# Performance work log

Hardware: AMD Instinct MI355X
Metric: run time of the kernel (lower is better)

The kernel has to match this reference:

```python
import jax, jax.numpy as jnp
import numpy as np

N = 50000   # nodes
E = 800000  # edges
H = 128     # hidden_dim
K = 4       # Chebyshev order
EPS_BN = 1e-5
EPS_L2 = 1e-12


def setup_inputs() -> dict:
    key = jax.random.key(0)
    ks = jax.random.split(key, 8)
    x = jax.random.normal(ks[0], (N, 3), dtype=jnp.float32)
    edge_index = jax.random.randint(ks[1], (2, E), 0, N, dtype=jnp.int32)

    def lin(k, fi, fo):
        s = 1.0 / np.sqrt(fi)
        return jax.random.uniform(k, (fi, fo), jnp.float32, -s, s)

    def cheb_params(k, fi, fo):
        kk = jax.random.split(k, K)
        W = jnp.stack([lin(kk[i], fi, fo) for i in range(K)])  # [K, fi, fo]
        b = jnp.zeros((fo,), jnp.float32)
        return W, b

    W1, b1 = cheb_params(ks[2], 3, H)
    W2, b2 = cheb_params(ks[3], H, H)
    W3, b3 = cheb_params(ks[4], H, H)
    W4, b4 = cheb_params(ks[5], H, H)
    Wr = lin(ks[6], H, 3)
    br = jnp.zeros((3,), jnp.float32)
    ones = jnp.ones((H,), jnp.float32)
    zeros = jnp.zeros((H,), jnp.float32)
    return {
        'x': x, 'edge_index': edge_index,
        'W1': W1, 'b1': b1, 'W2': W2, 'b2': b2,
        'W3': W3, 'b3': b3, 'W4': W4, 'b4': b4,
        'g1': ones, 'be1': zeros, 'g2': ones, 'be2': zeros,
        'g3': ones, 'be3': zeros, 'Wr': Wr, 'br': br,
    }


def _prop(h, src, dst, norm):
    # one sparse Laplacian application: out[dst] += norm * h[src]
    return jax.ops.segment_sum(norm[:, None] * h[src], dst, num_segments=N)


def _cheb(h, src, dst, norm, W, b):
    # PyG ChebConv with sym normalization, lambda_max=2 -> L_hat edge weights
    # are -D^-1/2 A D^-1/2 with zero diagonal (encoded in norm).
    out = h @ W[0]
    Tx0, Tx1 = h, _prop(h, src, dst, norm)
    out = out + Tx1 @ W[1]
    for k in range(2, W.shape[0]):
        Tx2 = 2.0 * _prop(Tx1, src, dst, norm) - Tx0
        out = out + Tx2 @ W[k]
        Tx0, Tx1 = Tx1, Tx2
    return out + b


def _bn(h, g, b):
    # BatchNorm1d in training mode: batch stats over node dim, biased var
    m = h.mean(axis=0)
    v = h.var(axis=0)
    return g * (h - m) * jax.lax.rsqrt(v + EPS_BN) + b


def reference(x, edge_index, W1, b1, W2, b2, W3, b3, W4, b4,
              g1, be1, g2, be2, g3, be3, Wr, br):
    src, dst = edge_index[0], edge_index[1]
    deg = jax.ops.segment_sum(jnp.ones((E,), jnp.float32), src, num_segments=N)
    dinv = jnp.where(deg > 0, jax.lax.rsqrt(jnp.maximum(deg, 1.0)), 0.0)
    norm = -dinv[src] * dinv[dst]

    h = _bn(jax.nn.leaky_relu(_cheb(x, src, dst, norm, W1, b1)), g1, be1)
    h = _bn(jax.nn.leaky_relu(_cheb(h, src, dst, norm, W2, b2)), g2, be2)
    h = _bn(jax.nn.relu(_cheb(h, src, dst, norm, W3, b3)), g3, be3)
    h = _cheb(h, src, dst, norm, W4, b4)
    # F.normalize(p=2, dim=1)
    h = h / jnp.maximum(jnp.linalg.norm(h, axis=1, keepdims=True), EPS_L2)
    return h @ Wr + br
```

## Files before the change

### kernel.cpp

```cpp
#include <hip/hip_runtime.h>
#include <hip/hip_fp16.h>

#define HD 128

typedef __attribute__((ext_vector_type(8))) _Float16 f16x8;
typedef __attribute__((ext_vector_type(4))) float f32x4;
typedef unsigned int u32;

struct h4s { __half2 a, b; };
struct h8s { __half2 a, b, c, d; };

__device__ __forceinline__ float lrelu(float x, float s) { return x > 0.f ? x : s * x; }

__device__ __forceinline__ float2 bn_coeff(const float* st, const float* g,
                                           const float* be, float invn, int f) {
  float m = st[f] * invn;
  float v = st[HD + f] * invn - m * m;
  float sc = g[f] * rsqrtf(v + 1e-5f);
  return make_float2(sc, be[f] - m * sc);
}

__global__ void k_edge_count(const int* __restrict__ src, const int* __restrict__ dst,
                             int* __restrict__ degc, int* __restrict__ cnt,
                             int* __restrict__ ledge, int E) {
  int e = blockIdx.x * blockDim.x + threadIdx.x;
  if (e < E) {
    atomicAdd(&degc[src[e]], 1);
    ledge[e] = atomicAdd(&cnt[dst[e]], 1);
  }
}

__global__ __launch_bounds__(1024) void k_scan1(const int* __restrict__ cnt,
                                                int* __restrict__ rowptr,
                                                int* __restrict__ bsums,
                                                float* __restrict__ stats, int n) {
  if (blockIdx.x == 0 && threadIdx.x < 6 * HD) stats[threadIdx.x] = 0.f;
  __shared__ int buf[1024];
  int i = blockIdx.x * 1024 + threadIdx.x;
  int v = (i < n) ? cnt[i] : 0;
  buf[threadIdx.x] = v;
  __syncthreads();
  for (int o = 1; o < 1024; o <<= 1) {
    int t = (threadIdx.x >= (unsigned)o) ? buf[threadIdx.x - o] : 0;
    __syncthreads();
    buf[threadIdx.x] += t;
    __syncthreads();
  }
  if (i < n) rowptr[i] = buf[threadIdx.x] - v;
  if (threadIdx.x == 1023) bsums[blockIdx.x] = buf[1023];
}

__global__ __launch_bounds__(1024) void k_scan3(int* __restrict__ rowptr,
                                                const int* __restrict__ bsums,
                                                const int* __restrict__ degc,
                                                float* __restrict__ dinv, int n, int Etot,
                                                int nb) {
  __shared__ int blockoff;
  if (nb <= 64) {
    if (threadIdx.x < 64) {
      int lane = threadIdx.x;
      int v = (lane < nb) ? bsums[lane] : 0;
      int inc = v;
#pragma unroll
      for (int o = 1; o < 64; o <<= 1) {
        int t = __shfl_up(inc, o, 64);
        if (lane >= o) inc += t;
      }
      if (lane == (int)blockIdx.x) blockoff = inc - v;
    }
  } else if (threadIdx.x == 0) {
    int sum = 0;
    for (int t = 0; t < (int)blockIdx.x; ++t) sum += bsums[t];
    blockoff = sum;
  }
  __syncthreads();
  int i = blockIdx.x * 1024 + threadIdx.x;
  if (i < n) {
    rowptr[i] += blockoff;
    int dg = degc[i];
    dinv[i] = dg > 0 ? rsqrtf((float)dg) : 0.f;
  }
  if (i == 0) rowptr[n] = Etot;
}

__global__ void k_fill(const int* __restrict__ src, const int* __restrict__ dst,
                       const int* __restrict__ ledge, const int* __restrict__ rowptr,
                       const float* __restrict__ dinv, uint2* __restrict__ cw, int E) {
  int e = blockIdx.x * blockDim.x + threadIdx.x;
  if (e < E) {
    int s = src[e], d = dst[e];
    int p = rowptr[d] + ledge[e];
    cw[p] = make_uint2((u32)s, __float_as_uint(-dinv[s] * dinv[d]));
  }
}

__global__ void k_prop3(const int* __restrict__ rowptr, const uint2* __restrict__ cw,
                        const float* __restrict__ Hs, const float* __restrict__ Sub,
                        float* __restrict__ Out, float scale, int n) {
  int r = blockIdx.x * blockDim.x + threadIdx.x;
  if (r >= n) return;
  int b = rowptr[r], e = rowptr[r + 1];
  float a0 = 0.f, a1 = 0.f, a2 = 0.f;
  for (int j = b; j < e; ++j) {
    uint2 m = cw[j];
    int s = (int)m.x;
    float w = __uint_as_float(m.y);
    a0 = fmaf(w, Hs[s * 3 + 0], a0);
    a1 = fmaf(w, Hs[s * 3 + 1], a1);
    a2 = fmaf(w, Hs[s * 3 + 2], a2);
  }
  float r0 = scale * a0, r1 = scale * a1, r2 = scale * a2;
  if (Sub) { r0 -= Sub[r * 3 + 0]; r1 -= Sub[r * 3 + 1]; r2 -= Sub[r * 3 + 2]; }
  Out[r * 3 + 0] = r0; Out[r * 3 + 1] = r1; Out[r * 3 + 2] = r2;
}

template <int PHI>
__global__ __launch_bounds__(256) void k_prop128(
    const int* __restrict__ rowptr, const uint2* __restrict__ cw,
    const __half* __restrict__ Ph, const __half* __restrict__ Sub,
    __half* __restrict__ Outh, float scale, int n, float invn,
    const float* __restrict__ gst, const float* __restrict__ gg, const float* __restrict__ gbe,
    const float* __restrict__ sst, const float* __restrict__ sg, const float* __restrict__ sbe,
    float slope) {
  int r = blockIdx.x * 4 + (int)(threadIdx.x >> 6);
  int lane = threadIdx.x & 63;
  if (r >= n) return;
  int b = rowptr[r], e = rowptr[r + 1];
  int fo = (lane & 15) << 3;
  int eo = lane >> 4;
  float a0 = 0.f, a1 = 0.f, a2 = 0.f, a3 = 0.f;
  float a4 = 0.f, a5 = 0.f, a6 = 0.f, a7 = 0.f, ws = 0.f;
  for (int j = b; j < e; j += 16) {
    h8s h[4];
    float w[4];
#pragma unroll
    for (int q = 0; q < 4; ++q) {
      int idx = j + q * 4 + eo;
      uint2 m = (idx < e) ? cw[idx] : make_uint2(0u, 0u);
      w[q] = __uint_as_float(m.y);
      h[q] = *(const h8s*)&Ph[(size_t)m.x * HD + fo];
    }
#pragma unroll
    for (int q = 0; q < 4; ++q) {
      float2 f0 = __half22float2(h[q].a);
      float2 f1 = __half22float2(h[q].b);
      float2 f2 = __half22float2(h[q].c);
      float2 f3 = __half22float2(h[q].d);
      if (PHI) {
        f0.x = lrelu(f0.x, slope); f0.y = lrelu(f0.y, slope);
        f1.x = lrelu(f1.x, slope); f1.y = lrelu(f1.y, slope);
        f2.x = lrelu(f2.x, slope); f2.y = lrelu(f2.y, slope);
        f3.x = lrelu(f3.x, slope); f3.y = lrelu(f3.y, slope);
        ws += w[q];
      }
      a0 = fmaf(w[q], f0.x, a0); a1 = fmaf(w[q], f0.y, a1);
      a2 = fmaf(w[q], f1.x, a2); a3 = fmaf(w[q], f1.y, a3);
      a4 = fmaf(w[q], f2.x, a4); a5 = fmaf(w[q], f2.y, a5);
      a6 = fmaf(w[q], f3.x, a6); a7 = fmaf(w[q], f3.y, a7);
    }
  }
#pragma unroll
  for (int mk = 16; mk <= 32; mk <<= 1) {
    a0 += __shfl_xor(a0, mk, 64); a1 += __shfl_xor(a1, mk, 64);
    a2 += __shfl_xor(a2, mk, 64); a3 += __shfl_xor(a3, mk, 64);
    a4 += __shfl_xor(a4, mk, 64); a5 += __shfl_xor(a5, mk, 64);
    a6 += __shfl_xor(a6, mk, 64); a7 += __shfl_xor(a7, mk, 64);
    if (PHI) ws += __shfl_xor(ws, mk, 64);
  }
  if (eo == 0) {
    float av[8] = {a0, a1, a2, a3, a4, a5, a6, a7};
    if (PHI) {
#pragma unroll
      for (int i = 0; i < 8; ++i) {
        float2 c = bn_coeff(gst, gg, gbe, invn, fo + i);
        av[i] = fmaf(av[i], c.x, ws * c.y);
      }
    }
#pragma unroll
    for (int i = 0; i < 8; ++i) av[i] *= scale;
    if (Sub) {
      h8s sh8 = *(const h8s*)&Sub[(size_t)r * HD + fo];
      float sv[8];
      float2 s0 = __half22float2(sh8.a), s1 = __half22float2(sh8.b);
      float2 s2 = __half22float2(sh8.c), s3 = __half22float2(sh8.d);
      sv[0] = s0.x; sv[1] = s0.y; sv[2] = s1.x; sv[3] = s1.y;
      sv[4] = s2.x; sv[5] = s2.y; sv[6] = s3.x; sv[7] = s3.y;
      if (sst != nullptr) {
#pragma unroll
        for (int i = 0; i < 8; ++i) {
          float2 d = bn_coeff(sst, sg, sbe, invn, fo + i);
          sv[i] = fmaf(lrelu(sv[i], slope), d.x, d.y);
        }
      }
#pragma unroll
      for (int i = 0; i < 8; ++i) av[i] -= sv[i];
    }
    h8s ho;
    ho.a = __float22half2_rn(make_float2(av[0], av[1]));
    ho.b = __float22half2_rn(make_float2(av[2], av[3]));
    ho.c = __float22half2_rn(make_float2(av[4], av[5]));
    ho.d = __float22half2_rn(make_float2(av[6], av[7]));
    *(h8s*)&Outh[(size_t)r * HD + fo] = ho;
  }
}

__global__ __launch_bounds__(128) void k_l1gemm(
    const float* __restrict__ X, const float* __restrict__ T1, const float* __restrict__ T2,
    const float* __restrict__ T3, const float* __restrict__ W1, const float* __restrict__ b1,
    __half* __restrict__ Outh, float* __restrict__ bnsum, float* __restrict__ bnsq,
    float slope, int n, int rpb) {
  int j = threadIdx.x;
  float w[12];
#pragma unroll
  for (int t = 0; t < 4; ++t)
#pragma unroll
    for (int c = 0; c < 3; ++c) w[t * 3 + c] = W1[(t * 3 + c) * HD + j];
  float bj = b1[j];
  int r0 = blockIdx.x * rpb, r1 = min(r0 + rpb, n);
  float s = 0.f, q = 0.f;
  for (int r = r0; r < r1; ++r) {
    float acc = bj;
#pragma unroll
    for (int c = 0; c < 3; ++c) {
      acc = fmaf(X [r * 3 + c], w[0 + c], acc);
      acc = fmaf(T1[r * 3 + c], w[3 + c], acc);
      acc = fmaf(T2[r * 3 + c], w[6 + c], acc);
      acc = fmaf(T3[r * 3 + c], w[9 + c], acc);
    }
    Outh[(size_t)r * HD + j] = __float2half(acc);
    float a = lrelu(acc, slope);
    s += a;
    q = fmaf(a, a, q);
  }
  atomicAdd(&bnsum[j], s);
  atomicAdd(&bnsq[j], q);
}

__global__ void k_wsplit3(const float* __restrict__ W2, const float* __restrict__ W3,
                          const float* __restrict__ W4, uint4* __restrict__ Whi,
                          uint4* __restrict__ Wlo) {
  int flat = blockIdx.x * 256 + threadIdx.x;
  int wsel = flat >> 13;
  int f = flat & 8191;
  const float* W = (wsel == 0) ? W2 : (wsel == 1) ? W3 : W4;
  int n = f & 127, K8 = f >> 7;
  int chunk = K8 >> 2, g = K8 & 3;
  f16x8 hv, lv;
#pragma unroll
  for (int i = 0; i < 8; ++i) {
    int k = chunk * 32 + ((i >> 2) << 4) + g * 4 + (i & 3);
    float v = W[(size_t)k * HD + n];
    _Float16 hh = (_Float16)v;
    _Float16 hl = (_Float16)(v - (float)hh);
    hv[i] = hh;
    lv[i] = hl;
  }
  int slot = chunk * 512 + (n >> 4) * 64 + g * 16 + (n & 15);
  Whi[wsel * 8192 + slot] = *(uint4*)&hv;
  Wlo[wsel * 8192 + slot] = *(uint4*)&lv;
}

__global__ __launch_bounds__(256) void k_gemm4m(
    const __half* __restrict__ T0, const __half* __restrict__ T1,
    const __half* __restrict__ T2, const __half* __restrict__ T3,
    const uint4* __restrict__ Whi, const uint4* __restrict__ Wlo,
    const float* __restrict__ bias, __half* __restrict__ OUTh,
    float* bnsum, float* bnsq, float stat_slope,
    const float* __restrict__ gst, const float* __restrict__ gg,
    const float* __restrict__ gbe, float invn, float phi_slope,
    const float* __restrict__ Wr, const float* __restrict__ br, float* __restrict__ outp,
    int nrows) {
  __shared__ __half sA[2048];
  __shared__ __half sWh[4096], sWl[4096];
  __shared__ float redS[128], redQ[128];
  __shared__ float fss[64];
  __shared__ float fob[64][3];

  int tid = threadIdx.x;
  int lane = tid & 63, w = tid >> 6, wr = w >> 1, wc = w & 1;
  int g = (tid >> 4) & 3;
  int ri = tid & 15;
  int row0 = blockIdx.x * 64;
  int arow = row0 + w * 16 + ri;
  bool aval = arow < nrows;

  f32x4 zero = {0.f, 0.f, 0.f, 0.f};
  f32x4 acc[2][4];
#pragma unroll
  for (int mi = 0; mi < 2; ++mi)
#pragma unroll
    for (int nj = 0; nj < 4; ++nj) acc[mi][nj] = zero;

  if (tid < 128) { redS[tid] = 0.f; redQ[tid] = 0.f; }
  if (tid < 64) { fss[tid] = 0.f; fob[tid][0] = 0.f; fob[tid][1] = 0.f; fob[tid][2] = 0.f; }

  for (int chunk = 0; chunk < 16; ++chunk) {
    const __half* Ts = (chunk < 4) ? T0 : (chunk < 8) ? T1 : (chunk < 12) ? T2 : T3;
    int kc = chunk & 3;
    h4s va, vb;
    *(uint2*)&va = make_uint2(0u, 0u);
    *(uint2*)&vb = make_uint2(0u, 0u);
    if (aval) {
      const __half* ap = Ts + (size_t)arow * HD + kc * 32 + g * 4;
      va = *(const h4s*)ap;
      vb = *(const h4s*)(ap + 16);
    }
    size_t wbase = (size_t)chunk * 512;
    uint4 wh0 = Whi[wbase + tid], wh1 = Whi[wbase + 256 + tid];
    uint4 wl0 = Wlo[wbase + tid], wl1 = Wlo[wbase + 256 + tid];

    __syncthreads();

    if (gst != nullptr && chunk < 4) {
      float fv[8];
      float2 f0 = __half22float2(va.a), f1 = __half22float2(va.b);
      float2 f2 = __half22float2(vb.a), f3 = __half22float2(vb.b);
      fv[0] = f0.x; fv[1] = f0.y; fv[2] = f1.x; fv[3] = f1.y;
      fv[4] = f2.x; fv[5] = f2.y; fv[6] = f3.x; fv[7] = f3.y;
#pragma unroll
      for (int i = 0; i < 8; ++i) {
        int f = kc * 32 + g * 4 + (i & 3) + ((i >> 2) << 4);
        float2 cs = bn_coeff(gst, gg, gbe, invn, f);
        fv[i] = fmaf(lrelu(fv[i], phi_slope), cs.x, cs.y);
      }
      va.a = __float22half2_rn(make_float2(fv[0], fv[1]));
      va.b = __float22half2_rn(make_float2(fv[2], fv[3]));
      vb.a = __float22half2_rn(make_float2(fv[4], fv[5]));
      vb.b = __float22half2_rn(make_float2(fv[6], fv[7]));
    }
    *(h4s*)&sA[tid * 8] = va;
    *(h4s*)&sA[tid * 8 + 4] = vb;
    *(uint4*)&sWh[tid * 8] = wh0;
    *(uint4*)&sWh[(256 + tid) * 8] = wh1;
    *(uint4*)&sWl[tid * 8] = wl0;
    *(uint4*)&sWl[(256 + tid) * 8] = wl1;
    __syncthreads();

    f16x8 a[2], bh[4], bl[4];
#pragma unroll
    for (int mi = 0; mi < 2; ++mi)
      a[mi] = *(const f16x8*)&sA[((wr * 2 + mi) * 64 + lane) * 8];
#pragma unroll
    for (int nj = 0; nj < 4; ++nj) {
      bh[nj] = *(const f16x8*)&sWh[((wc * 4 + nj) * 64 + lane) * 8];
      bl[nj] = *(const f16x8*)&sWl[((wc * 4 + nj) * 64 + lane) * 8];
    }
#pragma unroll
    for (int mi = 0; mi < 2; ++mi)
#pragma unroll
      for (int nj = 0; nj < 4; ++nj) {
        acc[mi][nj] = __builtin_amdgcn_mfma_f32_16x16x32_f16(a[mi], bh[nj], acc[mi][nj], 0, 0, 0);
        acc[mi][nj] = __builtin_amdgcn_mfma_f32_16x16x32_f16(a[mi], bl[nj], acc[mi][nj], 0, 0, 0);
      }
  }

  int l4 = (lane >> 4) * 4, ni = lane & 15;

  if (outp == nullptr) {
    bool stats = (bnsum != nullptr);
#pragma unroll
    for (int nj = 0; nj < 4; ++nj) {
      int c = wc * 64 + nj * 16 + ni;
      float bcol = bias[c];
      float s = 0.f, q = 0.f;
#pragma unroll
      for (int mi = 0; mi < 2; ++mi)
#pragma unroll
        for (int j = 0; j < 4; ++j) {
          int row = row0 + (wr * 2 + mi) * 16 + l4 + j;
          if (row < nrows) {
            float v = acc[mi][nj][j] + bcol;
            OUTh[(size_t)row * HD + c] = __float2half(v);
            if (stats) {
              float a = lrelu(v, stat_slope);
              s += a;
              q = fmaf(a, a, q);
            }
          }
        }
      if (stats) {
        s += __shfl_xor(s, 16, 64);
        s += __shfl_xor(s, 32, 64);
        q += __shfl_xor(q, 16, 64);
        q += __shfl_xor(q, 32, 64);
        if (lane < 16) {
          atomicAdd(&redS[c], s);
          atomicAdd(&redQ[c], q);
        }
      }
    }
    if (stats) {
      __syncthreads();
      if (tid < 128) {
        atomicAdd(&bnsum[tid], redS[tid]);
        atomicAdd(&bnsq[tid], redQ[tid]);
      }
    }
  } else {
    __syncthreads();
    float ss8[2][4];
#pragma unroll
    for (int mi = 0; mi < 2; ++mi)
#pragma unroll
      for (int j = 0; j < 4; ++j) ss8[mi][j] = 0.f;
#pragma unroll
    for (int nj = 0; nj < 4; ++nj) {
      int c = wc * 64 + nj * 16 + ni;
      float bcol = bias[c];
#pragma unroll
      for (int mi = 0; mi < 2; ++mi)
#pragma unroll
        for (int j = 0; j < 4; ++j) {
          float v = acc[mi][nj][j] + bcol;
          ss8[mi][j] = fmaf(v, v, ss8[mi][j]);
        }
    }
#pragma unroll
    for (int mk = 1; mk <= 8; mk <<= 1)
#pragma unroll
      for (int mi = 0; mi < 2; ++mi)
#pragma unroll
        for (int j = 0; j < 4; ++j) ss8[mi][j] += __shfl_xor(ss8[mi][j], mk, 64);
    if (ni == 0) {
#pragma unroll
      for (int mi = 0; mi < 2; ++mi)
#pragma unroll
        for (int j = 0; j < 4; ++j)
          atomicAdd(&fss[(wr * 2 + mi) * 16 + l4 + j], ss8[mi][j]);
    }
    __syncthreads();
    if (tid < 64) fss[tid] = 1.f / fmaxf(sqrtf(fss[tid]), 1e-12f);
    __syncthreads();
#pragma unroll
    for (int mi = 0; mi < 2; ++mi)
#pragma unroll
      for (int j = 0; j < 4; ++j) {
        int rl = (wr * 2 + mi) * 16 + l4 + j;
        float inv = fss[rl];
        float o0 = 0.f, o1 = 0.f, o2 = 0.f;
#pragma unroll
        for (int nj = 0; nj < 4; ++nj) {
          int c = wc * 64 + nj * 16 + ni;
          float v = (acc[mi][nj][j] + bias[c]) * inv;
          o0 = fmaf(v, Wr[c * 3 + 0], o0);
          o1 = fmaf(v, Wr[c * 3 + 1], o1);
          o2 = fmaf(v, Wr[c * 3 + 2], o2);
        }
#pragma unroll
        for (int mk = 1; mk <= 8; mk <<= 1) {
          o0 += __shfl_xor(o0, mk, 64);
          o1 += __shfl_xor(o1, mk, 64);
          o2 += __shfl_xor(o2, mk, 64);
        }
        if (ni == 0) {
          atomicAdd(&fob[rl][0], o0);
          atomicAdd(&fob[rl][1], o1);
          atomicAdd(&fob[rl][2], o2);
        }
      }
    __syncthreads();
    if (tid < 64) {
      int row = row0 + tid;
      if (row < nrows) {
        outp[row * 3 + 0] = fob[tid][0] + br[0];
        outp[row * 3 + 1] = fob[tid][1] + br[1];
        outp[row * 3 + 2] = fob[tid][2] + br[2];
      }
    }
  }
}

extern "C" void kernel_launch(void* const* d_in, const int* in_sizes, int n_in,
                              void* d_out, int out_size, void* d_ws, size_t ws_size,
                              hipStream_t stream) {
  const float* x  = (const float*)d_in[0];
  const int*   ei = (const int*)d_in[1];
  const float* W1 = (const float*)d_in[2];
  const float* b1 = (const float*)d_in[3];
  const float* W2 = (const float*)d_in[4];
  const float* b2 = (const float*)d_in[5];
  const float* W3 = (const float*)d_in[6];
  const float* b3 = (const float*)d_in[7];
  const float* W4 = (const float*)d_in[8];
  const float* b4 = (const float*)d_in[9];
  const float* g1 = (const float*)d_in[10];
  const float* be1= (const float*)d_in[11];
  const float* g2 = (const float*)d_in[12];
  const float* be2= (const float*)d_in[13];
  const float* g3 = (const float*)d_in[14];
  const float* be3= (const float*)d_in[15];
  const float* Wr = (const float*)d_in[16];
  const float* br = (const float*)d_in[17];

  const int N = in_sizes[0] / 3;
  const int E = in_sizes[1] / 2;
  const int* src = ei;
  const int* dst = ei + E;
  float* out = (float*)d_out;
  const float invn = 1.0f / (float)N;

  char* wp = (char*)d_ws;
  size_t used = 0;
  auto alloc = [&](size_t bytes) -> void* {
    void* p = (void*)(wp + used);
    used += (bytes + 255) & ~(size_t)255;
    return p;
  };
  int*   deg2   = (int*)alloc((size_t)2 * N * 4);
  int*   rowptr = (int*)alloc((size_t)(N + 1) * 4);
  float* dinv   = (float*)alloc((size_t)N * 4);
  int*   bsums  = (int*)alloc(256 * 4);
  int*   ledge  = (int*)alloc((size_t)E * 4);
  uint2* cw     = (uint2*)alloc((size_t)E * 8);
  float* t1     = (float*)alloc((size_t)N * 3 * 4);
  float* t2     = (float*)alloc((size_t)N * 3 * 4);
  float* t3     = (float*)alloc((size_t)N * 3 * 4);
  __half* phA   = (__half*)alloc((size_t)N * HD * 2);
  __half* phB   = (__half*)alloc((size_t)N * HD * 2);
  __half* phC   = (__half*)alloc((size_t)N * HD * 2);
  __half* phD   = (__half*)alloc((size_t)N * HD * 2);
  float* stats  = (float*)alloc(6 * HD * 4);
  uint4* Whi3   = (uint4*)alloc(3 * 8192 * 16);
  uint4* Wlo3   = (uint4*)alloc(3 * 8192 * 16);
  if (used > ws_size) return;

  int* degc = deg2;
  int* cnt  = deg2 + N;
  float* st1 = stats + 0 * HD;
  float* st2 = stats + 2 * HD;
  float* st3 = stats + 4 * HD;

  const int eb = (E + 255) / 256;
  const int nb = (N + 255) / 256;
  const int pb = (N + 3) / 4;
  const int sb = (N + 1023) / 1024;
  const int gbm = (N + 63) / 64;

  hipMemsetAsync(deg2, 0, (size_t)2 * N * 4, stream);
  k_edge_count<<<eb, 256, 0, stream>>>(src, dst, degc, cnt, ledge, E);
  k_scan1<<<sb, 1024, 0, stream>>>(cnt, rowptr, bsums, stats, N);
  k_scan3<<<sb, 1024, 0, stream>>>(rowptr, bsums, degc, dinv, N, E, sb);
  k_fill<<<eb, 256, 0, stream>>>(src, dst, ledge, rowptr, dinv, cw, E);
  k_wsplit3<<<96, 256, 0, stream>>>(W2, W3, W4, Whi3, Wlo3);

  k_prop3<<<nb, 256, 0, stream>>>(rowptr, cw, x, nullptr, t1, 1.f, N);
  k_prop3<<<nb, 256, 0, stream>>>(rowptr, cw, t1, x, t2, 2.f, N);
  k_prop3<<<nb, 256, 0, stream>>>(rowptr, cw, t2, t1, t3, 2.f, N);
  k_l1gemm<<<(N + 255) / 256, 128, 0, stream>>>(x, t1, t2, t3, W1, b1, phA,
                                                st1, st1 + HD, 0.01f, N, 256);

  auto cheb_layer = [&](const uint4* Whi, const uint4* Wlo, const float* bk,
                        const float* gst, const float* gg, const float* gbe, float phi_slope,
                        float* so, float stat_slope,
                        const float* Wrp, const float* brp, float* outp) {
    k_prop128<1><<<pb, 256, 0, stream>>>(rowptr, cw, phA, nullptr, phB, 1.f, N, invn,
                                         gst, gg, gbe, nullptr, nullptr, nullptr, phi_slope);
    k_prop128<0><<<pb, 256, 0, stream>>>(rowptr, cw, phB, phA, phC, 2.f, N, invn,
                                         nullptr, nullptr, nullptr, gst, gg, gbe, phi_slope);
    k_prop128<0><<<pb, 256, 0, stream>>>(rowptr, cw, phC, phB, phD, 2.f, N, invn,
                                         nullptr, nullptr, nullptr, nullptr, nullptr, nullptr,
                                         0.f);
    k_gemm4m<<<gbm, 256, 0, stream>>>(phA, phB, phC, phD, Whi, Wlo, bk, phA,
                                      so, so ? so + HD : nullptr, stat_slope,
                                      gst, gg, gbe, invn, phi_slope,
                                      Wrp, brp, outp, N);
  };

  cheb_layer(Whi3, Wlo3, b2, st1, g1, be1, 0.01f, st2, 0.01f, nullptr, nullptr, nullptr);
  cheb_layer(Whi3 + 8192, Wlo3 + 8192, b3, st2, g2, be2, 0.01f, st3, 0.0f,
             nullptr, nullptr, nullptr);
  cheb_layer(Whi3 + 16384, Wlo3 + 16384, b4, st3, g3, be3, 0.0f, nullptr, 0.0f, Wr, br, out);
}
```

Before: 693.6 us.

## Store hidden features in 32-column chunked layout and propagate per chunk

Hidden activations move from row-major [N,128] to four column-chunked [4][N][32] fp16 planes. Each sparse propagation now runs as four launches, one per chunk, so the gather working set per pass (N×64 bytes) is small enough to stay in cache. The GEMM loads and stores and the layer-1 output are rewritten for the new layout, and edge and sub loads and the output store use nontemporal hints. In exchange the edge list and row pointers are read four times per propagation and there are more kernel launches.

```diff
diff --git a/kernel.cpp b/kernel.cpp
--- a/kernel.cpp
+++ b/kernel.cpp
@@ -6,11 +6,21 @@
 typedef __attribute__((ext_vector_type(8))) _Float16 f16x8;
 typedef __attribute__((ext_vector_type(4))) float f32x4;
 typedef unsigned int u32;
+typedef unsigned long long u64;
 
 struct h4s { __half2 a, b; };
-struct h8s { __half2 a, b, c, d; };
 
 __device__ __forceinline__ float lrelu(float x, float s) { return x > 0.f ? x : s * x; }
+
+__device__ __forceinline__ float2 u32f2(u32 v) {
+  __half2 h;
+  *reinterpret_cast<u32*>(&h) = v;
+  return __half22float2(h);
+}
+__device__ __forceinline__ u32 f2u32(float2 f) {
+  __half2 h = __float22half2_rn(f);
+  return *reinterpret_cast<u32*>(&h);
+}
 
 __device__ __forceinline__ float2 bn_coeff(const float* st, const float* g,
                                            const float* be, float invn, int f) {
@@ -115,10 +125,10 @@
 }
 
 template <int PHI>
-__global__ __launch_bounds__(256) void k_prop128(
-    const int* __restrict__ rowptr, const uint2* __restrict__ cw,
-    const __half* __restrict__ Ph, const __half* __restrict__ Sub,
-    __half* __restrict__ Outh, float scale, int n, float invn,
+__global__ __launch_bounds__(256) void k_prop128c(
+    const int* __restrict__ rowptr, const u64* __restrict__ cw8,
+    const __half* __restrict__ PhC, const __half* __restrict__ SubC,
+    __half* __restrict__ OutC, float scale, int n, int pass, float invn,
     const float* __restrict__ gst, const float* __restrict__ gg, const float* __restrict__ gbe,
     const float* __restrict__ sst, const float* __restrict__ sg, const float* __restrict__ sbe,
     float slope) {
@@ -126,88 +136,82 @@
   int lane = threadIdx.x & 63;
   if (r >= n) return;
   int b = rowptr[r], e = rowptr[r + 1];
-  int fo = (lane & 15) << 3;
-  int eo = lane >> 4;
-  float a0 = 0.f, a1 = 0.f, a2 = 0.f, a3 = 0.f;
-  float a4 = 0.f, a5 = 0.f, a6 = 0.f, a7 = 0.f, ws = 0.f;
-  for (int j = b; j < e; j += 16) {
-    h8s h[4];
+  int fo = (lane & 7) << 2;
+  int eo = lane >> 3;
+  const __half* srcC = PhC + (size_t)pass * n * 32;
+  float a0 = 0.f, a1 = 0.f, a2 = 0.f, a3 = 0.f, ws = 0.f;
+  for (int j = b; j < e; j += 32) {
+    u64 hv[4];
     float w[4];
 #pragma unroll
     for (int q = 0; q < 4; ++q) {
-      int idx = j + q * 4 + eo;
-      uint2 m = (idx < e) ? cw[idx] : make_uint2(0u, 0u);
-      w[q] = __uint_as_float(m.y);
-      h[q] = *(const h8s*)&Ph[(size_t)m.x * HD + fo];
+      int idx = j + q * 8 + eo;
+      u64 m = (idx < e) ? __builtin_nontemporal_load(&cw8[idx]) : 0ull;
+      w[q] = __uint_as_float((u32)(m >> 32));
+      u32 s = (u32)m;
+      hv[q] = *(const u64*)&srcC[(size_t)s * 32 + fo];
     }
 #pragma unroll
     for (int q = 0; q < 4; ++q) {
-      float2 f0 = __half22float2(h[q].a);
-      float2 f1 = __half22float2(h[q].b);
-      float2 f2 = __half22float2(h[q].c);
-      float2 f3 = __half22float2(h[q].d);
+      float2 f0 = u32f2((u32)hv[q]);
+      float2 f1 = u32f2((u32)(hv[q] >> 32));
       if (PHI) {
         f0.x = lrelu(f0.x, slope); f0.y = lrelu(f0.y, slope);
         f1.x = lrelu(f1.x, slope); f1.y = lrelu(f1.y, slope);
-        f2.x = lrelu(f2.x, slope); f2.y = lrelu(f2.y, slope);
-        f3.x = lrelu(f3.x, slope); f3.y = lrelu(f3.y, slope);
         ws += w[q];
       }
-      a0 = fmaf(w[q], f0.x, a0); a1 = fmaf(w[q], f0.y, a1);
-      a2 = fmaf(w[q], f1.x, a2); a3 = fmaf(w[q], f1.y, a3);
-      a4 = fmaf(w[q], f2.x, a4); a5 = fmaf(w[q], f2.y, a5);
-      a6 = fmaf(w[q], f3.x, a6); a7 = fmaf(w[q], f3.y, a7);
-    }
-  }
-#pragma unroll
-  for (int mk = 16; mk <= 32; mk <<= 1) {
-    a0 += __shfl_xor(a0, mk, 64); a1 += __shfl_xor(a1, mk, 64);
-    a2 += __shfl_xor(a2, mk, 64); a3 += __shfl_xor(a3, mk, 64);
-    a4 += __shfl_xor(a4, mk, 64); a5 += __shfl_xor(a5, mk, 64);
-    a6 += __shfl_xor(a6, mk, 64); a7 += __shfl_xor(a7, mk, 64);
+      a0 = fmaf(w[q], f0.x, a0);
+      a1 = fmaf(w[q], f0.y, a1);
+      a2 = fmaf(w[q], f1.x, a2);
+      a3 = fmaf(w[q], f1.y, a3);
+    }
+  }
+#pragma unroll
+  for (int mk = 8; mk <= 32; mk <<= 1) {
+    a0 += __shfl_xor(a0, mk, 64);
+    a1 += __shfl_xor(a1, mk, 64);
+    a2 += __shfl_xor(a2, mk, 64);
+    a3 += __shfl_xor(a3, mk, 64);
     if (PHI) ws += __shfl_xor(ws, mk, 64);
   }
   if (eo == 0) {
-    float av[8] = {a0, a1, a2, a3, a4, a5, a6, a7};
+    int fg = pass * 32 + fo;
+    float av[4] = {a0, a1, a2, a3};
     if (PHI) {
 #pragma unroll
-      for (int i = 0; i < 8; ++i) {
-        float2 c = bn_coeff(gst, gg, gbe, invn, fo + i);
+      for (int i = 0; i < 4; ++i) {
+        float2 c = bn_coeff(gst, gg, gbe, invn, fg + i);
         av[i] = fmaf(av[i], c.x, ws * c.y);
       }
     }
 #pragma unroll
-    for (int i = 0; i < 8; ++i) av[i] *= scale;
-    if (Sub) {
-      h8s sh8 = *(const h8s*)&Sub[(size_t)r * HD + fo];
-      float sv[8];
-      float2 s0 = __half22float2(sh8.a), s1 = __half22float2(sh8.b);
-      float2 s2 = __half22float2(sh8.c), s3 = __half22float2(sh8.d);
-      sv[0] = s0.x; sv[1] = s0.y; sv[2] = s1.x; sv[3] = s1.y;
-      sv[4] = s2.x; sv[5] = s2.y; sv[6] = s3.x; sv[7] = s3.y;
+    for (int i = 0; i < 4; ++i) av[i] *= scale;
+    size_t off = (size_t)pass * n * 32 + (size_t)r * 32 + fo;
+    if (SubC) {
+      u64 sv = __builtin_nontemporal_load((const u64*)&SubC[off]);
+      float2 s0 = u32f2((u32)sv);
+      float2 s1 = u32f2((u32)(sv >> 32));
+      float svf[4] = {s0.x, s0.y, s1.x, s1.y};
       if (sst != nullptr) {
 #pragma unroll
-        for (int i = 0; i < 8; ++i) {
-          float2 d = bn_coeff(sst, sg, sbe, invn, fo + i);
-          sv[i] = fmaf(lrelu(sv[i], slope), d.x, d.y);
-        }
-      }
-#pragma unroll
-      for (int i = 0; i < 8; ++i) av[i] -= sv[i];
-    }
-    h8s ho;
-    ho.a = __float22half2_rn(make_float2(av[0], av[1]));
-    ho.b = __float22half2_rn(make_float2(av[2], av[3]));
-    ho.c = __float22half2_rn(make_float2(av[4], av[5]));
-    ho.d = __float22half2_rn(make_float2(av[6], av[7]));
-    *(h8s*)&Outh[(size_t)r * HD + fo] = ho;
+        for (int i = 0; i < 4; ++i) {
+          float2 d = bn_coeff(sst, sg, sbe, invn, fg + i);
+          svf[i] = fmaf(lrelu(svf[i], slope), d.x, d.y);
+        }
+      }
+#pragma unroll
+      for (int i = 0; i < 4; ++i) av[i] -= svf[i];
+    }
+    u64 outv = (u64)f2u32(make_float2(av[0], av[1])) |
+               ((u64)f2u32(make_float2(av[2], av[3])) << 32);
+    __builtin_nontemporal_store(outv, (u64*)&OutC[off]);
   }
 }
 
 __global__ __launch_bounds__(128) void k_l1gemm(
     const float* __restrict__ X, const float* __restrict__ T1, const float* __restrict__ T2,
     const float* __restrict__ T3, const float* __restrict__ W1, const float* __restrict__ b1,
-    __half* __restrict__ Outh, float* __restrict__ bnsum, float* __restrict__ bnsq,
+    __half* __restrict__ OutC, float* __restrict__ bnsum, float* __restrict__ bnsq,
     float slope, int n, int rpb) {
   int j = threadIdx.x;
   float w[12];
@@ -216,6 +220,7 @@
 #pragma unroll
     for (int c = 0; c < 3; ++c) w[t * 3 + c] = W1[(t * 3 + c) * HD + j];
   float bj = b1[j];
+  size_t obase = (size_t)(j >> 5) * n * 32 + (j & 31);
   int r0 = blockIdx.x * rpb, r1 = min(r0 + rpb, n);
   float s = 0.f, q = 0.f;
   for (int r = r0; r < r1; ++r) {
@@ -227,7 +232,7 @@
       acc = fmaf(T2[r * 3 + c], w[6 + c], acc);
       acc = fmaf(T3[r * 3 + c], w[9 + c], acc);
     }
-    Outh[(size_t)r * HD + j] = __float2half(acc);
+    OutC[obase + (size_t)r * 32] = __float2half(acc);
     float a = lrelu(acc, slope);
     s += a;
     q = fmaf(a, a, q);
@@ -301,7 +306,7 @@
     *(uint2*)&va = make_uint2(0u, 0u);
     *(uint2*)&vb = make_uint2(0u, 0u);
     if (aval) {
-      const __half* ap = Ts + (size_t)arow * HD + kc * 32 + g * 4;
+      const __half* ap = Ts + ((size_t)kc * nrows + arow) * 32 + g * 4;
       va = *(const h4s*)ap;
       vb = *(const h4s*)(ap + 16);
     }
@@ -362,6 +367,7 @@
     for (int nj = 0; nj < 4; ++nj) {
       int c = wc * 64 + nj * 16 + ni;
       float bcol = bias[c];
+      size_t obase = (size_t)(c >> 5) * nrows * 32 + (c & 31);
       float s = 0.f, q = 0.f;
 #pragma unroll
       for (int mi = 0; mi < 2; ++mi)
@@ -370,7 +376,7 @@
           int row = row0 + (wr * 2 + mi) * 16 + l4 + j;
           if (row < nrows) {
             float v = acc[mi][nj][j] + bcol;
-            OUTh[(size_t)row * HD + c] = __float2half(v);
+            OUTh[obase + (size_t)row * 32] = __float2half(v);
             if (stats) {
               float a = lrelu(v, stat_slope);
               s += a;
@@ -549,17 +555,22 @@
   k_l1gemm<<<(N + 255) / 256, 128, 0, stream>>>(x, t1, t2, t3, W1, b1, phA,
                                                 st1, st1 + HD, 0.01f, N, 256);
 
+  const u64* cw8 = (const u64*)cw;
+
   auto cheb_layer = [&](const uint4* Whi, const uint4* Wlo, const float* bk,
                         const float* gst, const float* gg, const float* gbe, float phi_slope,
                         float* so, float stat_slope,
                         const float* Wrp, const float* brp, float* outp) {
-    k_prop128<1><<<pb, 256, 0, stream>>>(rowptr, cw, phA, nullptr, phB, 1.f, N, invn,
-                                         gst, gg, gbe, nullptr, nullptr, nullptr, phi_slope);
-    k_prop128<0><<<pb, 256, 0, stream>>>(rowptr, cw, phB, phA, phC, 2.f, N, invn,
-                                         nullptr, nullptr, nullptr, gst, gg, gbe, phi_slope);
-    k_prop128<0><<<pb, 256, 0, stream>>>(rowptr, cw, phC, phB, phD, 2.f, N, invn,
-                                         nullptr, nullptr, nullptr, nullptr, nullptr, nullptr,
-                                         0.f);
+    for (int p = 0; p < 4; ++p)
+      k_prop128c<1><<<pb, 256, 0, stream>>>(rowptr, cw8, phA, nullptr, phB, 1.f, N, p, invn,
+                                            gst, gg, gbe, nullptr, nullptr, nullptr, phi_slope);
+    for (int p = 0; p < 4; ++p)
+      k_prop128c<0><<<pb, 256, 0, stream>>>(rowptr, cw8, phB, phA, phC, 2.f, N, p, invn,
+                                            nullptr, nullptr, nullptr, gst, gg, gbe, phi_slope);
+    for (int p = 0; p < 4; ++p)
+      k_prop128c<0><<<pb, 256, 0, stream>>>(rowptr, cw8, phC, phB, phD, 2.f, N, p, invn,
+                                            nullptr, nullptr, nullptr, nullptr, nullptr,
+                                            nullptr, 0.f);
     k_gemm4m<<<gbm, 256, 0, stream>>>(phA, phB, phC, phD, Whi, Wlo, bk, phA,
                                       so, so ? so + HD : nullptr, stat_slope,
                                       gst, gg, gbe, invn, phi_slope,
```

After: 1.328 ms. 1.91x slower.
